# Optimization experiments

Measured on AMD Instinct MI355X. Metric: run time of the kernel, lower is better.

The kernel has to match this reference:

```python
import jax, jax.numpy as jnp
import numpy as np

ANCHORS = np.array([[10,13],[16,30],[33,23],[30,61],[62,45],[59,119],[116,90],[156,198],[373,326]], dtype=np.float32)
IMAGE_SIZE = 640
N_CLASSES = 80
MAX_BOXES = 150
SCORE_THRESH = 0.9
IOU_THRESH = 0.1
BATCH = 16


def setup_inputs() -> dict:
    key = jax.random.key(0)
    k0, k1, k2 = jax.random.split(key, 3)
    # scale logits so a realistic number of scores exceed the 0.9 threshold
    p0 = jax.random.normal(k0, (BATCH, 20, 20, 255), dtype=jnp.float32) * 2.5
    p1 = jax.random.normal(k1, (BATCH, 40, 40, 255), dtype=jnp.float32) * 2.5
    p2 = jax.random.normal(k2, (BATCH, 80, 80, 255), dtype=jnp.float32) * 2.5
    return {"p0": p0, "p1": p1, "p2": p2}


def _decode(fm, anchors):
    # fm: [B, g, g, 3*(5+C)] -> boxes [B, g*g*3, 4] (cx,cy,w,h), conf [B,N,1], prob [B,N,C]
    b, g = fm.shape[0], fm.shape[1]
    ratio = IMAGE_SIZE / g  # square image -> ratio_x == ratio_y
    fm = fm.reshape(b, g, g, 3, 5 + N_CLASSES)
    ctr, sz, conf, prob = jnp.split(fm, [2, 4, 5], axis=-1)
    gx, gy = jnp.meshgrid(jnp.arange(g), jnp.arange(g))  # 'xy' indexing, as tf.meshgrid
    off = jnp.stack([gx, gy], axis=-1).astype(fm.dtype)[:, :, None, :]  # [g,g,1,2]
    ctr = (jax.nn.sigmoid(ctr) + off) * ratio
    # (anchor / ratio) * ratio == anchor
    sz = jnp.exp(sz) * jnp.asarray(anchors, fm.dtype)  # [B,g,g,3,2] * [3,2]
    boxes = jnp.concatenate([ctr, sz], axis=-1).reshape(b, g * g * 3, 4)
    conf = jax.nn.sigmoid(conf).reshape(b, g * g * 3, 1)
    prob = jax.nn.sigmoid(prob).reshape(b, g * g * 3, N_CLASSES)
    return boxes, conf, prob


def _pairwise_iou(b):  # b: [K,4] in xyxy
    area = (b[:, 2] - b[:, 0]) * (b[:, 3] - b[:, 1])
    lt = jnp.maximum(b[:, None, :2], b[None, :, :2])
    rb = jnp.minimum(b[:, None, 2:], b[None, :, 2:])
    wh = jnp.clip(rb - lt, 0.0)
    inter = wh[..., 0] * wh[..., 1]
    return inter / (area[:, None] + area[None, :] - inter + 1e-9)


def _nms_class(boxes, scores):
    # boxes [N,4], scores [N]: threshold, take top MAX_BOXES candidates, greedy NMS.
    masked = jnp.where(scores > SCORE_THRESH, scores, -1.0)
    top_s, top_i = jax.lax.top_k(masked, MAX_BOXES)  # sorted desc, matches tf NMS ordering
    cand = boxes[top_i]
    valid = top_s > SCORE_THRESH
    iou = _pairwise_iou(cand)  # [K,K]
    idx = jnp.arange(MAX_BOXES)

    def body(suppressed, i):
        keep_i = valid[i] & ~suppressed[i]
        suppressed = suppressed | (keep_i & (iou[i] > IOU_THRESH) & (idx > i))
        return suppressed, keep_i

    _, keep = jax.lax.scan(body, jnp.zeros(MAX_BOXES, bool), idx)
    return top_i, top_s, keep


def _per_image(boxes, cls_scores):
    # boxes [N,4] xyxy, cls_scores [N,C]
    top_i, top_s, keep = jax.vmap(lambda s: _nms_class(boxes, s))(cls_scores.T)  # [C,K]
    labels = jnp.broadcast_to(jnp.arange(N_CLASSES)[:, None], top_i.shape)
    fi = top_i.reshape(-1)
    fs = jnp.where(keep.reshape(-1), top_s.reshape(-1), -1.0)
    fl = labels.reshape(-1)
    fk = keep.reshape(-1)
    sel_s, sel = jax.lax.top_k(fs, MAX_BOXES)  # final top-k across all classes
    v = fk[sel]
    out_boxes = jnp.where(v[:, None], boxes[fi[sel]], -1.0)
    out_scores = jnp.where(v, sel_s, -1.0)
    out_labels = jnp.where(v, fl[sel], -1).astype(jnp.int32)
    return out_boxes, out_scores, out_labels


def _forward(p0, p1, p2):
    parts = [(p0, ANCHORS[6:9]), (p1, ANCHORS[3:6]), (p2, ANCHORS[0:3])]
    boxes_l, conf_l, prob_l = [], [], []
    for fm, anc in parts:
        bx, cf, pr = _decode(fm, anc)
        boxes_l.append(bx); conf_l.append(cf); prob_l.append(pr)
    boxes = jnp.concatenate(boxes_l, axis=1)  # [B,N,4] cxcywh
    conf = jnp.concatenate(conf_l, axis=1)
    prob = jnp.concatenate(prob_l, axis=1)
    cx, cy, w, h = jnp.split(boxes, 4, axis=-1)
    boxes = jnp.concatenate([cx - w / 2, cy - h / 2, cx + w / 2, cy + h / 2], axis=-1)
    scores = conf * prob  # [B,N,C]
    return jax.vmap(_per_image)(boxes, scores)


def reference(p0, p1, p2):
    return _forward(p0, p1, p2)
```

## Files before the change

### kernel.cpp

```cpp
#include <hip/hip_runtime.h>
#include <stdint.h>

#define NCLS 80
#define MAXB 150
#define BATCH 16
#define NANCH 25200
#define SEGS 4
#define SEGCAP 512
#define CAP2 12000
#define NBINS 411
#define SELCAP 2048
#define WSEL 256
#define NREC_ALL 403200
#define CPAD 16

typedef unsigned long long u64;
typedef unsigned int u32;
typedef float f4 __attribute__((ext_vector_type(4)));
typedef f4 f4u __attribute__((aligned(4)));

__device__ __forceinline__ float sigm(float x) { return 1.0f / (1.0f + expf(-x)); }

__device__ __forceinline__ float iou_ref(float4 rb_, float ra, float4 cb, float ca) {
  float ltx = fmaxf(rb_.x, cb.x);
  float lty = fmaxf(rb_.y, cb.y);
  float rbx = fminf(rb_.z, cb.z);
  float rby = fminf(rb_.w, cb.w);
  float iw = fmaxf(rbx - ltx, 0.f);
  float ih = fmaxf(rby - lty, 0.f);
  float inter = iw * ih;
  return inter / (ra + ca - inter + 1e-9f);
}

__global__ __launch_bounds__(256) void decode_kernel(
    const float* __restrict__ p0, const float* __restrict__ p1,
    const float* __restrict__ p2, float* __restrict__ boxes_ws,
    u64* __restrict__ cand_keys, int* __restrict__ cand_cnt) {
  __shared__ int hcnt;
  __shared__ u32 hW[256];
  __shared__ float hthr[256];
  __shared__ float hcs[256];
  int tid = threadIdx.x;
  if (tid == 0) hcnt = 0;
  __syncthreads();
  int W = blockIdx.x * 256 + tid;
  int lvl, b, r;
  if (W < 19200) { lvl = 0; b = W / 1200; r = W - b * 1200; }
  else if (W < 96000) { int V = W - 19200; lvl = 1; b = V / 4800; r = V - b * 4800; }
  else { int V = W - 96000; lvl = 2; b = V / 19200; r = V - b * 19200; }
  const int gtab[3] = {20, 40, 80};
  const float rtab[3] = {32.f, 16.f, 8.f};
  const int nbt[3] = {0, 1200, 6000};
  const float awt[3][3] = {{116.f, 156.f, 373.f}, {30.f, 62.f, 59.f}, {10.f, 16.f, 33.f}};
  const float aht[3][3] = {{90.f, 198.f, 326.f}, {61.f, 45.f, 119.f}, {13.f, 30.f, 23.f}};
  const float* fm = (lvl == 0) ? p0 : ((lvl == 1) ? p1 : p2);
  int g = gtab[lvl];
  const float* p = fm + ((size_t)b * (g * g * 3) + r) * 85;
  float tc = p[4];
  float cs = sigm(tc);
  if (cs > 0.9f) {
    f4 h = *(const f4u*)p;
    int cell = r / 3, a = r - 3 * cell;
    int yy = cell / g, xx = cell - yy * g;
    float ratio = rtab[lvl];
    float cx = (sigm(h.x) + (float)xx) * ratio;
    float cy = (sigm(h.y) + (float)yy) * ratio;
    float w = expf(h.z) * awt[lvl][a];
    float hh = expf(h.w) * aht[lvl][a];
    int n = nbt[lvl] + r;
    reinterpret_cast<float4*>(boxes_ws)[(size_t)b * NANCH + n] = make_float4(
        cx - w * 0.5f, cy - hh * 0.5f, cx + w * 0.5f, cy + hh * 0.5f);
    float t = 0.9f / cs;
    float ratio2 = t / (1.0f - t);
    float thr = logf(ratio2) - (1e-3f + 4e-7f * ratio2);
    int pos = atomicAdd(&hcnt, 1);
    hW[pos] = (u32)W;
    hthr[pos] = thr;
    hcs[pos] = cs;
  }
  __syncthreads();
  int H = hcnt;
  int idx = tid / 20, slot = tid - idx * 20;
  if (tid < 240) {
    for (int base = 0; base < H; base += 12) {
      int e = base + idx;
      if (e < H) {
        u32 Wr = hW[e];
        float thr = hthr[e];
        float cs = hcs[e];
        int lv2, b2, r2;
        const float* fm2;
        if (Wr < 19200u) { lv2 = 0; b2 = Wr / 1200u; r2 = Wr - b2 * 1200u; fm2 = p0; }
        else if (Wr < 96000u) { u32 V = Wr - 19200u; lv2 = 1; b2 = V / 4800u; r2 = V - b2 * 4800u; fm2 = p1; }
        else { u32 V = Wr - 96000u; lv2 = 2; b2 = V / 19200u; r2 = V - b2 * 19200u; fm2 = p2; }
        const int lbase[3] = {0, 19200, 96000};
        const float* pr = fm2 + (size_t)(Wr - (u32)lbase[lv2]) * 85;
        f4 v = *(const f4u*)(pr + 5 + 4 * slot);
        u32 n = (u32)nbt[lv2] + (u32)r2;
        u32 nkey = 0xFFFFFFFFu - n;
        int seg = (int)(Wr & (SEGS - 1));
#pragma unroll
        for (int k = 0; k < 4; ++k) {
          if (v[k] > thr) {
            float s = cs * sigm(v[k]);
            if (s > 0.9f) {
              int c = 4 * slot + k;
              int bc = b2 * NCLS + c;
              int pos = atomicAdd(&cand_cnt[(bc * SEGS + seg) * CPAD], 1);
              if (pos < SEGCAP)
                cand_keys[((size_t)bc * SEGS + seg) * SEGCAP + pos] =
                    ((u64)__float_as_uint(s) << 32) | nkey;
            }
          }
        }
      }
    }
  }
}

__global__ __launch_bounds__(64) void nms_kernel(
    const u64* __restrict__ cand_keys, const int* __restrict__ cand_cnt,
    const float* __restrict__ boxes_ws,
    u64* __restrict__ img_keys, int* __restrict__ img_cnt) {
  __shared__ u64 sel[WSEL + 8];
  __shared__ u64 slot[MAXB];
  __shared__ float4 sbox[MAXB];
  __shared__ float sarea[MAXB];
  __shared__ u64 adjm[MAXB][3];
  __shared__ u32 hist[NBINS];
  int bc = blockIdx.x;
  int b = bc / NCLS, c = bc - b * NCLS;
  int lane = threadIdx.x;
  u64 ltm = (1ull << lane) - 1;
  int cnt[SEGS];
  int count = 0;
#pragma unroll
  for (int s = 0; s < SEGS; ++s) {
    int v = cand_cnt[(bc * SEGS + s) * CPAD];
    cnt[s] = (v > SEGCAP) ? SEGCAP : v;
    count += cnt[s];
  }
  const u64* seg_base = cand_keys + (size_t)bc * SEGS * SEGCAP;
  for (int i = lane; i < NBINS; i += 64) hist[i] = 0;
  for (int i = lane; i < MAXB; i += 64) slot[i] = 0;
#pragma unroll
  for (int s = 0; s < SEGS; ++s)
    for (int i = lane; i < cnt[s]; i += 64) {
      u64 k = seg_base[s * SEGCAP + i];
      atomicAdd(&hist[((u32)(k >> 32) - 0x3F666000u) >> 12], 1u);
    }
  __threadfence_block();
  int target = (count < MAXB) ? count : MAXB;
  u32 bsum[7];
  u32 csum = 0;
  int chunk = lane * 7;
#pragma unroll
  for (int m = 0; m < 7; ++m) {
    int j = chunk + m;
    u32 hv = (j < NBINS) ? hist[j] : 0u;
    bsum[m] = hv;
    csum += hv;
  }
  u32 S = csum;
#pragma unroll
  for (int off = 1; off < 64; off <<= 1) {
    u32 o = __shfl_down(S, off);
    if (lane + off < 64) S += o;
  }
  u32 Snext = S - csum;
  bool win = (S >= (u32)target) && (Snext < (u32)target);
  u64 wmask = __ballot(win);
  int T = NBINS;
  u32 Cge = 0;
  if (wmask) {
    int Tc = 0;
    u32 Cc = 0;
    if (win) {
      u32 acc = Snext;
#pragma unroll
      for (int m = 6; m >= 0; --m) {
        acc += bsum[m];
        if (acc >= (u32)target) { Tc = chunk + m; Cc = acc; break; }
      }
    }
    int wl = __ffsll(wmask) - 1;
    T = __shfl(Tc, wl);
    Cge = __shfl(Cc, wl);
  }
  if (Cge <= WSEL) {
    int C = 0;
#pragma unroll
    for (int s = 0; s < SEGS; ++s)
      for (int i0 = 0; i0 < cnt[s]; i0 += 64) {
        int i = i0 + lane;
        bool in = false;
        u64 k = 0;
        if (i < cnt[s]) {
          k = seg_base[s * SEGCAP + i];
          in = (int)(((u32)(k >> 32) - 0x3F666000u) >> 12) >= T;
        }
        u64 m = __ballot(in);
        if (in) sel[C + (int)__popcll(m & ltm)] = k;
        C += (int)__popcll(m);
      }
    int C8 = (C + 7) & ~7;
    for (int j = C + lane; j < C8; j += 64) sel[j] = 0;
    __threadfence_block();
    for (int i = lane; i < C; i += 64) {
      u64 k = sel[i];
      int rank = 0;
      for (int j = 0; j < C8; j += 8) {
        rank += (int)(sel[j] > k) + (int)(sel[j + 1] > k) + (int)(sel[j + 2] > k) +
                (int)(sel[j + 3] > k) + (int)(sel[j + 4] > k) + (int)(sel[j + 5] > k) +
                (int)(sel[j + 6] > k) + (int)(sel[j + 7] > k);
      }
      if (rank < MAXB) slot[rank] = k;
    }
  } else {
#pragma unroll
    for (int s = 0; s < SEGS; ++s)
      for (int i = lane; i < cnt[s]; i += 64) {
        u64 k = seg_base[s * SEGCAP + i];
        int rank = 0;
        for (int s2 = 0; s2 < SEGS; ++s2)
          for (int j = 0; j < cnt[s2]; ++j)
            rank += (seg_base[s2 * SEGCAP + j] > k) ? 1 : 0;
        if (rank < MAXB) slot[rank] = k;
      }
  }
  __threadfence_block();
  float4 rb0, rb1, rb2;
  float ra0 = 0.f, ra1 = 0.f, ra2 = 0.f;
  rb0 = rb1 = rb2 = make_float4(0.f, 0.f, 0.f, 0.f);
#pragma unroll
  for (int w = 0; w < 3; ++w) {
    int j = lane + 64 * w;
    float4 bx = make_float4(0.f, 0.f, 0.f, 0.f);
    float ar = 0.f;
    if (j < MAXB && slot[j] != 0) {
      int n = (int)(0xFFFFFFFFu - (u32)(slot[j] & 0xFFFFFFFFu));
      bx = reinterpret_cast<const float4*>(boxes_ws)[(size_t)b * NANCH + n];
      ar = (bx.z - bx.x) * (bx.w - bx.y);
    }
    if (j < MAXB) { sbox[j] = bx; sarea[j] = ar; }
    if (w == 0) { rb0 = bx; ra0 = ar; }
    else if (w == 1) { rb1 = bx; ra1 = ar; }
    else { rb2 = bx; ra2 = ar; }
  }
  u64 valid0 = __ballot(slot[lane] != 0);
  u64 valid1 = __ballot(lane + 64 < MAXB && slot[lane + 64] != 0);
  u64 valid2 = __ballot(lane + 128 < MAXB && slot[lane + 128] != 0);
  __threadfence_block();
  int jb0 = (target < 64) ? target : 64;
  int jb1 = (target < 128) ? target : 128;
  int jb2 = target;
  u64 r0m0 = 0, r0m1 = 0, r0m2 = 0, r1m1 = 0, r1m2 = 0, r2m2 = 0;
  bool rv0 = (valid0 >> lane) & 1, rv1 = (valid1 >> lane) & 1,
       rv2 = (valid2 >> lane) & 1;
  if (rv0) {
    u64 bit = 1ull;
    for (int j = 0; j < jb0; ++j, bit <<= 1)
      if (j > lane && iou_ref(rb0, ra0, sbox[j], sarea[j]) > 0.1f) r0m0 |= bit;
    bit = 1ull;
    for (int j = 64; j < jb1; ++j, bit <<= 1)
      if (iou_ref(rb0, ra0, sbox[j], sarea[j]) > 0.1f) r0m1 |= bit;
    bit = 1ull;
    for (int j = 128; j < jb2; ++j, bit <<= 1)
      if (iou_ref(rb0, ra0, sbox[j], sarea[j]) > 0.1f) r0m2 |= bit;
  }
  if (rv1) {
    u64 bit = 1ull;
    for (int j = 64; j < jb1; ++j, bit <<= 1)
      if (j > lane + 64 && iou_ref(rb1, ra1, sbox[j], sarea[j]) > 0.1f) r1m1 |= bit;
    bit = 1ull;
    for (int j = 128; j < jb2; ++j, bit <<= 1)
      if (iou_ref(rb1, ra1, sbox[j], sarea[j]) > 0.1f) r1m2 |= bit;
  }
  if (rv2) {
    u64 bit = 1ull;
    for (int j = 128; j < jb2; ++j, bit <<= 1)
      if (j > lane + 128 && iou_ref(rb2, ra2, sbox[j], sarea[j]) > 0.1f) r2m2 |= bit;
  }
  if (lane < MAXB) { adjm[lane][0] = r0m0; adjm[lane][1] = r0m1; adjm[lane][2] = r0m2; }
  if (lane + 64 < MAXB) { adjm[lane + 64][0] = 0; adjm[lane + 64][1] = r1m1; adjm[lane + 64][2] = r1m2; }
  if (lane + 128 < MAXB) { adjm[lane + 128][0] = 0; adjm[lane + 128][1] = 0; adjm[lane + 128][2] = r2m2; }
  __threadfence_block();
  u64 sup0 = 0, sup1 = 0, sup2 = 0;
  {
    u64 bit = 1ull;
    int e0 = (target < 64) ? target : 64;
    for (int i = 0; i < e0; ++i, bit <<= 1)
      if (valid0 & ~sup0 & bit) { sup0 |= adjm[i][0]; sup1 |= adjm[i][1]; sup2 |= adjm[i][2]; }
    bit = 1ull;
    int e1 = (target < 128) ? target - 64 : 64;
    for (int i = 0; i < e1; ++i, bit <<= 1)
      if (valid1 & ~sup1 & bit) { sup1 |= adjm[i + 64][1]; sup2 |= adjm[i + 64][2]; }
    bit = 1ull;
    int e2 = target - 128;
    for (int i = 0; i < e2; ++i, bit <<= 1)
      if (valid2 & ~sup2 & bit) { sup2 |= adjm[i + 128][2]; }
  }
  u64 m0 = valid0 & ~sup0, m1 = valid1 & ~sup1, m2 = valid2 & ~sup2;
  int total = (int)(__popcll(m0) + __popcll(m1) + __popcll(m2));
  if (total > 0) {
    int base = 0;
    if (lane == 0) base = atomicAdd(&img_cnt[b * CPAD], total);
    base = __shfl(base, 0);
    int off0 = (int)__popcll(m0 & ltm);
    int off1 = (int)(__popcll(m0) + __popcll(m1 & ltm));
    int off2 = (int)(__popcll(m0) + __popcll(m1) + __popcll(m2 & ltm));
#pragma unroll
    for (int w = 0; w < 3; ++w) {
      u64 mw = (w == 0) ? m0 : ((w == 1) ? m1 : m2);
      if ((mw >> lane) & 1) {
        int j = lane + 64 * w;
        u64 k = slot[j];
        u32 e = (u32)(c * MAXB + j);
        u32 anchor = (u32)(0xFFFFFFFFu - (u32)(k & 0xFFFFFFFFu));
        int pos = base + ((w == 0) ? off0 : ((w == 1) ? off1 : off2));
        img_keys[(size_t)b * CAP2 + pos] =
            ((k >> 32) << 32) | ((u64)(0x3FFFu - e) << 15) | anchor;
      }
    }
  }
}

__global__ __launch_bounds__(1024) void final_kernel(
    const u64* __restrict__ img_keys, const int* __restrict__ img_cnt,
    const float* __restrict__ boxes_ws, float* __restrict__ out) {
  __shared__ u32 hist[NBINS];
  __shared__ u64 sel[SELCAP];
  __shared__ u64 slot[MAXB];
  __shared__ int sT, sCge, nsel;
  int b = blockIdx.x, tid = threadIdx.x;
  int L = img_cnt[b * CPAD];
  if (L > CAP2) L = CAP2;
  const u64* src = img_keys + (size_t)b * CAP2;
  for (int i = tid; i < NBINS; i += 1024) hist[i] = 0;
  if (tid < MAXB) slot[tid] = 0;
  if (tid == 0) nsel = 0;
  __syncthreads();
  for (int i = tid; i < L; i += 1024) {
    u32 hi = (u32)(src[i] >> 32);
    atomicAdd(&hist[(hi - 0x3F666000u) >> 12], 1u);
  }
  __syncthreads();
  if (tid < 64) {
    int lane = tid;
    int target = (L < MAXB) ? L : MAXB;
    u32 bsum[7];
    u32 csum = 0;
    int chunk = lane * 7;
#pragma unroll
    for (int m = 0; m < 7; ++m) {
      int j = chunk + m;
      u32 hv = (j < NBINS) ? hist[j] : 0u;
      bsum[m] = hv;
      csum += hv;
    }
    u32 S = csum;
#pragma unroll
    for (int off = 1; off < 64; off <<= 1) {
      u32 o = __shfl_down(S, off);
      if (lane + off < 64) S += o;
    }
    u32 Snext = S - csum;
    bool win = (S >= (u32)target) && (Snext < (u32)target);
    u64 wmask = __ballot(win);
    int T = NBINS;
    u32 Cge = 0;
    if (wmask) {
      int Tc = 0;
      u32 Cc = 0;
      if (win) {
        u32 acc = Snext;
#pragma unroll
        for (int m = 6; m >= 0; --m) {
          acc += bsum[m];
          if (acc >= (u32)target) { Tc = chunk + m; Cc = acc; break; }
        }
      }
      int wl = __ffsll(wmask) - 1;
      T = __shfl(Tc, wl);
      Cge = __shfl(Cc, wl);
    }
    if (lane == 0) { sT = T; sCge = (int)Cge; }
  }
  __syncthreads();
  int T = sT, cge = sCge;
  float* ob = out;
  float* osc = out + BATCH * MAXB * 4;
  float* olb = out + BATCH * MAXB * 5;
  if (cge <= SELCAP) {
    for (int i = tid; i < L; i += 1024) {
      u64 k = src[i];
      if ((int)(((u32)(k >> 32) - 0x3F666000u) >> 12) >= T) {
        int pos = atomicAdd(&nsel, 1);
        sel[pos] = k;
      }
    }
    __syncthreads();
    int C = nsel;
    for (int i = tid; i < C; i += 1024) {
      u64 k = sel[i];
      int rank = 0;
      for (int j = 0; j < C; ++j) rank += (sel[j] > k) ? 1 : 0;
      if (rank < MAXB) slot[rank] = k;
    }
    __syncthreads();
  } else {
    for (int i = tid; i < L; i += 1024) {
      u64 k = src[i];
      int rank = 0;
      for (int j = 0; j < L; ++j) rank += (src[j] > k) ? 1 : 0;
      if (rank < MAXB) slot[rank] = k;
    }
    __syncthreads();
  }
  if (tid < MAXB) {
    u64 k = slot[tid];
    float* q = ob + ((size_t)b * MAXB + tid) * 4;
    if (k) {
      u32 e = 0x3FFFu - (u32)((k >> 15) & 0x3FFFu);
      int c = (int)(e / MAXB);
      int anchor = (int)(k & 0x7FFFu);
      float4 bx = reinterpret_cast<const float4*>(boxes_ws)[(size_t)b * NANCH + anchor];
      q[0] = bx.x; q[1] = bx.y; q[2] = bx.z; q[3] = bx.w;
      osc[(size_t)b * MAXB + tid] = __uint_as_float((u32)(k >> 32));
      olb[(size_t)b * MAXB + tid] = (float)c;
    } else {
      q[0] = q[1] = q[2] = q[3] = -1.f;
      osc[(size_t)b * MAXB + tid] = -1.f;
      olb[(size_t)b * MAXB + tid] = -1.f;
    }
  }
}

extern "C" void kernel_launch(void* const* d_in, const int* in_sizes, int n_in,
                              void* d_out, int out_size, void* d_ws, size_t ws_size,
                              hipStream_t stream) {
  (void)in_sizes; (void)n_in; (void)out_size; (void)ws_size;
  const float* p0 = (const float*)d_in[0];
  const float* p1 = (const float*)d_in[1];
  const float* p2 = (const float*)d_in[2];
  char* ws = (char*)d_ws;
  float* boxes_ws = (float*)ws;
  int* cand_cnt = (int*)(ws + 6451200);
  int* img_cnt = (int*)(ws + 6778880);
  u64* cand_keys = (u64*)(ws + 6779904);
  u64* img_keys = (u64*)(ws + 27751424);

  hipMemsetAsync(cand_cnt, 0, (NCLS * BATCH * SEGS + BATCH) * CPAD * sizeof(int),
                 stream);

  decode_kernel<<<NREC_ALL / 256, 256, 0, stream>>>(
      p0, p1, p2, boxes_ws, cand_keys, cand_cnt);
  nms_kernel<<<BATCH * NCLS, 64, 0, stream>>>(cand_keys, cand_cnt, boxes_ws,
                                              img_keys, img_cnt);
  final_kernel<<<BATCH, 1024, 0, stream>>>(img_keys, img_cnt, boxes_ws, (float*)d_out);
}
```

Before: 131.8 us.

## Widen NMS kernel to 256 threads with flat pairwise IoU bitmask

Result: slower. 146.2 us (+11.0%).

```diff
diff --git a/kernel.cpp b/kernel.cpp
--- a/kernel.cpp
+++ b/kernel.cpp
@@ -118,7 +118,7 @@
   }
 }
 
-__global__ __launch_bounds__(64) void nms_kernel(
+__global__ __launch_bounds__(256) void nms_kernel(
     const u64* __restrict__ cand_keys, const int* __restrict__ cand_cnt,
     const float* __restrict__ boxes_ws,
     u64* __restrict__ img_keys, int* __restrict__ img_cnt) {
@@ -126,12 +126,13 @@
   __shared__ u64 slot[MAXB];
   __shared__ float4 sbox[MAXB];
   __shared__ float sarea[MAXB];
-  __shared__ u64 adjm[MAXB][3];
+  __shared__ u32 adjw[MAXB][5];
   __shared__ u32 hist[NBINS];
+  __shared__ u32 svalid[5];
+  __shared__ int sT, sCge, nsel, sBase;
   int bc = blockIdx.x;
   int b = bc / NCLS, c = bc - b * NCLS;
-  int lane = threadIdx.x;
-  u64 ltm = (1ull << lane) - 1;
+  int tid = threadIdx.x;
   int cnt[SEGS];
   int count = 0;
 #pragma unroll
@@ -140,73 +141,74 @@
     cnt[s] = (v > SEGCAP) ? SEGCAP : v;
     count += cnt[s];
   }
+  int target = (count < MAXB) ? count : MAXB;
   const u64* seg_base = cand_keys + (size_t)bc * SEGS * SEGCAP;
-  for (int i = lane; i < NBINS; i += 64) hist[i] = 0;
-  for (int i = lane; i < MAXB; i += 64) slot[i] = 0;
+  for (int i = tid; i < NBINS; i += 256) hist[i] = 0;
+  if (tid < MAXB) slot[tid] = 0;
+  for (int i = tid; i < MAXB * 5; i += 256) (&adjw[0][0])[i] = 0;
+  if (tid < 5) svalid[tid] = 0;
+  if (tid == 0) nsel = 0;
+  __syncthreads();
 #pragma unroll
   for (int s = 0; s < SEGS; ++s)
-    for (int i = lane; i < cnt[s]; i += 64) {
-      u64 k = seg_base[s * SEGCAP + i];
-      atomicAdd(&hist[((u32)(k >> 32) - 0x3F666000u) >> 12], 1u);
-    }
-  __threadfence_block();
-  int target = (count < MAXB) ? count : MAXB;
-  u32 bsum[7];
-  u32 csum = 0;
-  int chunk = lane * 7;
-#pragma unroll
-  for (int m = 0; m < 7; ++m) {
-    int j = chunk + m;
-    u32 hv = (j < NBINS) ? hist[j] : 0u;
-    bsum[m] = hv;
-    csum += hv;
-  }
-  u32 S = csum;
-#pragma unroll
-  for (int off = 1; off < 64; off <<= 1) {
-    u32 o = __shfl_down(S, off);
-    if (lane + off < 64) S += o;
-  }
-  u32 Snext = S - csum;
-  bool win = (S >= (u32)target) && (Snext < (u32)target);
-  u64 wmask = __ballot(win);
-  int T = NBINS;
-  u32 Cge = 0;
-  if (wmask) {
-    int Tc = 0;
-    u32 Cc = 0;
-    if (win) {
-      u32 acc = Snext;
-#pragma unroll
-      for (int m = 6; m >= 0; --m) {
-        acc += bsum[m];
-        if (acc >= (u32)target) { Tc = chunk + m; Cc = acc; break; }
-      }
-    }
-    int wl = __ffsll(wmask) - 1;
-    T = __shfl(Tc, wl);
-    Cge = __shfl(Cc, wl);
-  }
-  if (Cge <= WSEL) {
-    int C = 0;
+    for (int i = tid; i < cnt[s]; i += 256)
+      atomicAdd(&hist[((u32)(seg_base[s * SEGCAP + i] >> 32) - 0x3F666000u) >> 12], 1u);
+  __syncthreads();
+  if (tid < 64) {
+    int lane = tid;
+    u32 bsum[7];
+    u32 csum = 0;
+    int chunk = lane * 7;
+#pragma unroll
+    for (int m = 0; m < 7; ++m) {
+      int j = chunk + m;
+      u32 hv = (j < NBINS) ? hist[j] : 0u;
+      bsum[m] = hv;
+      csum += hv;
+    }
+    u32 S = csum;
+#pragma unroll
+    for (int off = 1; off < 64; off <<= 1) {
+      u32 o = __shfl_down(S, off);
+      if (lane + off < 64) S += o;
+    }
+    u32 Snext = S - csum;
+    bool win = (target > 0) && (S >= (u32)target) && (Snext < (u32)target);
+    u64 wmask = __ballot(win);
+    int T = NBINS;
+    u32 Cge = 0;
+    if (wmask) {
+      int Tc = 0;
+      u32 Cc = 0;
+      if (win) {
+        u32 acc = Snext;
+#pragma unroll
+        for (int m = 6; m >= 0; --m) {
+          acc += bsum[m];
+          if (acc >= (u32)target) { Tc = chunk + m; Cc = acc; break; }
+        }
+      }
+      int wl = __ffsll(wmask) - 1;
+      T = __shfl(Tc, wl);
+      Cge = __shfl(Cc, wl);
+    }
+    if (lane == 0) { sT = T; sCge = (int)Cge; }
+  }
+  __syncthreads();
+  int T = sT;
+  if (sCge <= WSEL) {
 #pragma unroll
     for (int s = 0; s < SEGS; ++s)
-      for (int i0 = 0; i0 < cnt[s]; i0 += 64) {
-        int i = i0 + lane;
-        bool in = false;
-        u64 k = 0;
-        if (i < cnt[s]) {
-          k = seg_base[s * SEGCAP + i];
-          in = (int)(((u32)(k >> 32) - 0x3F666000u) >> 12) >= T;
-        }
-        u64 m = __ballot(in);
-        if (in) sel[C + (int)__popcll(m & ltm)] = k;
-        C += (int)__popcll(m);
-      }
+      for (int i = tid; i < cnt[s]; i += 256) {
+        u64 k = seg_base[s * SEGCAP + i];
+        if ((int)(((u32)(k >> 32) - 0x3F666000u) >> 12) >= T) sel[atomicAdd(&nsel, 1)] = k;
+      }
+    __syncthreads();
+    int C = nsel;
     int C8 = (C + 7) & ~7;
-    for (int j = C + lane; j < C8; j += 64) sel[j] = 0;
-    __threadfence_block();
-    for (int i = lane; i < C; i += 64) {
+    for (int j = C + tid; j < C8; j += 256) sel[j] = 0;
+    __syncthreads();
+    for (int i = tid; i < C; i += 256) {
       u64 k = sel[i];
       int rank = 0;
       for (int j = 0; j < C8; j += 8) {
@@ -219,7 +221,7 @@
   } else {
 #pragma unroll
     for (int s = 0; s < SEGS; ++s)
-      for (int i = lane; i < cnt[s]; i += 64) {
+      for (int i = tid; i < cnt[s]; i += 256) {
         u64 k = seg_base[s * SEGCAP + i];
         int rank = 0;
         for (int s2 = 0; s2 < SEGS; ++s2)
@@ -228,99 +230,65 @@
         if (rank < MAXB) slot[rank] = k;
       }
   }
-  __threadfence_block();
-  float4 rb0, rb1, rb2;
-  float ra0 = 0.f, ra1 = 0.f, ra2 = 0.f;
-  rb0 = rb1 = rb2 = make_float4(0.f, 0.f, 0.f, 0.f);
-#pragma unroll
-  for (int w = 0; w < 3; ++w) {
-    int j = lane + 64 * w;
+  __syncthreads();
+  if (tid < MAXB) {
+    u64 k = slot[tid];
     float4 bx = make_float4(0.f, 0.f, 0.f, 0.f);
     float ar = 0.f;
-    if (j < MAXB && slot[j] != 0) {
-      int n = (int)(0xFFFFFFFFu - (u32)(slot[j] & 0xFFFFFFFFu));
+    if (k) {
+      int n = (int)(0xFFFFFFFFu - (u32)(k & 0xFFFFFFFFu));
       bx = reinterpret_cast<const float4*>(boxes_ws)[(size_t)b * NANCH + n];
       ar = (bx.z - bx.x) * (bx.w - bx.y);
-    }
-    if (j < MAXB) { sbox[j] = bx; sarea[j] = ar; }
-    if (w == 0) { rb0 = bx; ra0 = ar; }
-    else if (w == 1) { rb1 = bx; ra1 = ar; }
-    else { rb2 = bx; ra2 = ar; }
-  }
-  u64 valid0 = __ballot(slot[lane] != 0);
-  u64 valid1 = __ballot(lane + 64 < MAXB && slot[lane + 64] != 0);
-  u64 valid2 = __ballot(lane + 128 < MAXB && slot[lane + 128] != 0);
-  __threadfence_block();
-  int jb0 = (target < 64) ? target : 64;
-  int jb1 = (target < 128) ? target : 128;
-  int jb2 = target;
-  u64 r0m0 = 0, r0m1 = 0, r0m2 = 0, r1m1 = 0, r1m2 = 0, r2m2 = 0;
-  bool rv0 = (valid0 >> lane) & 1, rv1 = (valid1 >> lane) & 1,
-       rv2 = (valid2 >> lane) & 1;
-  if (rv0) {
-    u64 bit = 1ull;
-    for (int j = 0; j < jb0; ++j, bit <<= 1)
-      if (j > lane && iou_ref(rb0, ra0, sbox[j], sarea[j]) > 0.1f) r0m0 |= bit;
-    bit = 1ull;
-    for (int j = 64; j < jb1; ++j, bit <<= 1)
-      if (iou_ref(rb0, ra0, sbox[j], sarea[j]) > 0.1f) r0m1 |= bit;
-    bit = 1ull;
-    for (int j = 128; j < jb2; ++j, bit <<= 1)
-      if (iou_ref(rb0, ra0, sbox[j], sarea[j]) > 0.1f) r0m2 |= bit;
-  }
-  if (rv1) {
-    u64 bit = 1ull;
-    for (int j = 64; j < jb1; ++j, bit <<= 1)
-      if (j > lane + 64 && iou_ref(rb1, ra1, sbox[j], sarea[j]) > 0.1f) r1m1 |= bit;
-    bit = 1ull;
-    for (int j = 128; j < jb2; ++j, bit <<= 1)
-      if (iou_ref(rb1, ra1, sbox[j], sarea[j]) > 0.1f) r1m2 |= bit;
-  }
-  if (rv2) {
-    u64 bit = 1ull;
-    for (int j = 128; j < jb2; ++j, bit <<= 1)
-      if (j > lane + 128 && iou_ref(rb2, ra2, sbox[j], sarea[j]) > 0.1f) r2m2 |= bit;
-  }
-  if (lane < MAXB) { adjm[lane][0] = r0m0; adjm[lane][1] = r0m1; adjm[lane][2] = r0m2; }
-  if (lane + 64 < MAXB) { adjm[lane + 64][0] = 0; adjm[lane + 64][1] = r1m1; adjm[lane + 64][2] = r1m2; }
-  if (lane + 128 < MAXB) { adjm[lane + 128][0] = 0; adjm[lane + 128][1] = 0; adjm[lane + 128][2] = r2m2; }
-  __threadfence_block();
-  u64 sup0 = 0, sup1 = 0, sup2 = 0;
-  {
-    u64 bit = 1ull;
-    int e0 = (target < 64) ? target : 64;
-    for (int i = 0; i < e0; ++i, bit <<= 1)
-      if (valid0 & ~sup0 & bit) { sup0 |= adjm[i][0]; sup1 |= adjm[i][1]; sup2 |= adjm[i][2]; }
-    bit = 1ull;
-    int e1 = (target < 128) ? target - 64 : 64;
-    for (int i = 0; i < e1; ++i, bit <<= 1)
-      if (valid1 & ~sup1 & bit) { sup1 |= adjm[i + 64][1]; sup2 |= adjm[i + 64][2]; }
-    bit = 1ull;
-    int e2 = target - 128;
-    for (int i = 0; i < e2; ++i, bit <<= 1)
-      if (valid2 & ~sup2 & bit) { sup2 |= adjm[i + 128][2]; }
-  }
-  u64 m0 = valid0 & ~sup0, m1 = valid1 & ~sup1, m2 = valid2 & ~sup2;
-  int total = (int)(__popcll(m0) + __popcll(m1) + __popcll(m2));
-  if (total > 0) {
-    int base = 0;
-    if (lane == 0) base = atomicAdd(&img_cnt[b * CPAD], total);
-    base = __shfl(base, 0);
-    int off0 = (int)__popcll(m0 & ltm);
-    int off1 = (int)(__popcll(m0) + __popcll(m1 & ltm));
-    int off2 = (int)(__popcll(m0) + __popcll(m1) + __popcll(m2 & ltm));
-#pragma unroll
-    for (int w = 0; w < 3; ++w) {
-      u64 mw = (w == 0) ? m0 : ((w == 1) ? m1 : m2);
-      if ((mw >> lane) & 1) {
-        int j = lane + 64 * w;
-        u64 k = slot[j];
-        u32 e = (u32)(c * MAXB + j);
-        u32 anchor = (u32)(0xFFFFFFFFu - (u32)(k & 0xFFFFFFFFu));
-        int pos = base + ((w == 0) ? off0 : ((w == 1) ? off1 : off2));
-        img_keys[(size_t)b * CAP2 + pos] =
-            ((k >> 32) << 32) | ((u64)(0x3FFFu - e) << 15) | anchor;
-      }
+      atomicOr(&svalid[tid >> 5], 1u << (tid & 31));
+    }
+    sbox[tid] = bx;
+    sarea[tid] = ar;
+  }
+  __syncthreads();
+  for (int q = tid; q < MAXB * MAXB; q += 256) {
+    int i = q / MAXB, j = q - i * MAXB;
+    if (i < j && j < target) {
+      if (iou_ref(sbox[i], sarea[i], sbox[j], sarea[j]) > 0.1f)
+        atomicOr(&adjw[i][j >> 5], 1u << (j & 31));
+    }
+  }
+  __syncthreads();
+  u32 sup0 = 0, sup1 = 0, sup2 = 0, sup3 = 0, sup4 = 0;
+  u32 va0 = svalid[0], va1 = svalid[1], va2 = svalid[2], va3 = svalid[3],
+      va4 = svalid[4];
+  for (int i = 0; i < target; ++i) {
+    u32 bit = 1u << (i & 31);
+    int iw = i >> 5;
+    u32 viw = (iw == 0) ? va0 : ((iw == 1) ? va1 : ((iw == 2) ? va2 : ((iw == 3) ? va3 : va4)));
+    u32 siw = (iw == 0) ? sup0 : ((iw == 1) ? sup1 : ((iw == 2) ? sup2 : ((iw == 3) ? sup3 : sup4)));
+    if (viw & ~siw & bit) {
+      sup0 |= adjw[i][0];
+      sup1 |= adjw[i][1];
+      sup2 |= adjw[i][2];
+      sup3 |= adjw[i][3];
+      sup4 |= adjw[i][4];
+    }
+  }
+  u32 kp0 = va0 & ~sup0, kp1 = va1 & ~sup1, kp2 = va2 & ~sup2, kp3 = va3 & ~sup3,
+      kp4 = va4 & ~sup4;
+  int total = (int)(__popc(kp0) + __popc(kp1) + __popc(kp2) + __popc(kp3) + __popc(kp4));
+  if (tid == 0 && total > 0) sBase = atomicAdd(&img_cnt[b * CPAD], total);
+  __syncthreads();
+  if (tid < MAXB) {
+    int w = tid >> 5, bi = tid & 31;
+    u32 kw = (w == 0) ? kp0 : ((w == 1) ? kp1 : ((w == 2) ? kp2 : ((w == 3) ? kp3 : kp4)));
+    if ((kw >> bi) & 1) {
+      int pos = 0;
+      if (w > 0) pos += __popc(kp0);
+      if (w > 1) pos += __popc(kp1);
+      if (w > 2) pos += __popc(kp2);
+      if (w > 3) pos += __popc(kp3);
+      pos += __popc(kw & ((1u << bi) - 1u));
+      u64 k = slot[tid];
+      u32 e = (u32)(c * MAXB + tid);
+      u32 anchor = 0xFFFFFFFFu - (u32)(k & 0xFFFFFFFFu);
+      img_keys[(size_t)b * CAP2 + sBase + pos] =
+          ((k >> 32) << 32) | ((u64)(0x3FFFu - e) << 15) | anchor;
     }
   }
 }
@@ -365,7 +333,7 @@
       if (lane + off < 64) S += o;
     }
     u32 Snext = S - csum;
-    bool win = (S >= (u32)target) && (Snext < (u32)target);
+    bool win = (target > 0) && (S >= (u32)target) && (Snext < (u32)target);
     u64 wmask = __ballot(win);
     int T = NBINS;
     u32 Cge = 0;
@@ -455,7 +423,7 @@
 
   decode_kernel<<<NREC_ALL / 256, 256, 0, stream>>>(
       p0, p1, p2, boxes_ws, cand_keys, cand_cnt);
-  nms_kernel<<<BATCH * NCLS, 64, 0, stream>>>(cand_keys, cand_cnt, boxes_ws,
-                                              img_keys, img_cnt);
+  nms_kernel<<<BATCH * NCLS, 256, 0, stream>>>(cand_keys, cand_cnt, boxes_ws,
+                                               img_keys, img_cnt);
   final_kernel<<<BATCH, 1024, 0, stream>>>(img_keys, img_cnt, boxes_ws, (float*)d_out);
 }
```
